# Kernel optimization log

Measured on AMD Instinct MI355X. Metric: run time of the kernel, lower is better.

The kernel has to match this reference:

```python
import jax, jax.numpy as jnp
import numpy as np

N, E, F_IN, H, C = 100000, 1250000, 512, 64, 40
K = 2


def _lin_w(key, fan_out, fan_in):
    bound = 1.0 / np.sqrt(fan_in)
    return jax.random.uniform(key, (fan_out, fan_in), jnp.float32, -bound, bound)


def setup_inputs() -> dict:
    key = jax.random.key(0)
    ks = jax.random.split(key, 14)
    x = jax.random.normal(ks[0], (N, F_IN), dtype=jnp.float32)
    edge_index = jax.random.randint(ks[1], (2, E), 0, N, dtype=jnp.int64)
    inp = {
        "x": x,
        "edge_index": edge_index,
        "W_in": _lin_w(ks[2], H, F_IN),
        "b_in": jnp.zeros((H,), jnp.float32),
        "W1_0": _lin_w(ks[3], H, H),
        "W2_0": _lin_w(ks[4], H, H),
        "Wf_0": _lin_w(ks[5], H, H),
        "W1_1": _lin_w(ks[6], H, H),
        "W2_1": _lin_w(ks[7], H, H),
        "Wf_1": _lin_w(ks[8], H, H),
        "W_out": _lin_w(ks[9], C, H),
        "b_out": jnp.zeros((C,), jnp.float32),
    }
    return inp


def _step_conv(Q, row, col, W1, W2, Wf, n):
    # StepConv.forward with step == 0 (the only valid branch in the source)
    h3 = Q @ W1.T              # [N, H]
    h4 = Q @ W2.T              # [N, H]
    hloop = jax.nn.relu(Q @ Wf.T)
    # edge gate: s = sigmoid(-<h3[row], h4[col]>)  per edge
    s = jax.nn.sigmoid(-jnp.sum(h3[row] * h4[col], axis=1))  # [E]
    # propagate (source_to_target): scatter messages from row into col
    agg3 = jax.ops.segment_sum(s[:, None] * h3[row], col, num_segments=n)
    agg4 = jax.ops.segment_sum((1.0 - s)[:, None] * h4[row], col, num_segments=n)
    return hloop + agg3 - agg4


def reference(x, edge_index, W_in, b_in, W1_0, W2_0, Wf_0, W1_1, W2_1, Wf_1, W_out, b_out):
    n = x.shape[0]
    row, col = edge_index[0], edge_index[1]
    Q = x @ W_in.T + b_in
    for (W1, W2, Wf) in ((W1_0, W2_0, Wf_0), (W1_1, W2_1, Wf_1)):
        hq3 = _step_conv(Q, row, col, W1, W2, Wf, n)
        # F.normalize(p=2, dim=1), eps=1e-12
        Q = hq3 / jnp.maximum(jnp.linalg.norm(hq3, axis=1, keepdims=True), 1e-12)
    logits = Q @ W_out.T + b_out
    return jax.nn.log_softmax(logits, axis=1)
```

## Files before the change

### kernel.cpp

```cpp
#include <hip/hip_runtime.h>
#include <hip/hip_bf16.h>
#include <math.h>

#define H 64
#define FIN 512
#define COUT 40

typedef __attribute__((ext_vector_type(8))) short bf16x8;
typedef __attribute__((ext_vector_type(4))) float f32x4;

__device__ __forceinline__ unsigned short f2bf(float f) {
    union { float f; unsigned u; } v; v.f = f;
    unsigned r = v.u + 0x7FFF + ((v.u >> 16) & 1);
    return (unsigned short)(r >> 16);
}
__device__ __forceinline__ float bflo(unsigned u) { return __uint_as_float(u << 16); }
__device__ __forceinline__ float bfhi(unsigned u) { return __uint_as_float(u & 0xffff0000u); }

__global__ void k_pack(const float* __restrict__ W_in,
                       const float* __restrict__ W1_0, const float* __restrict__ W2_0,
                       const float* __restrict__ Wf_0,
                       const float* __restrict__ W1_1, const float* __restrict__ W2_1,
                       const float* __restrict__ Wf_1,
                       const float* __restrict__ W_out,
                       uint4* __restrict__ Bp, uint4* __restrict__ Bc0,
                       uint4* __restrict__ Bc1, uint4* __restrict__ Bo) {
    int t = blockIdx.x * blockDim.x + threadIdx.x;
    const float* src;
    uint4* dst;
    if (t < 4096) {
        int kb = t >> 6, n = t & 63;
        src = &W_in[n * FIN + kb * 8];
        dst = &Bp[t];
    } else if (t < 4096 + 1536) {
        int u = t - 4096;
        int j = u >> 9, kb = (u >> 6) & 7, n = u & 63;
        const float* W = (j == 0) ? W1_0 : (j == 1) ? W2_0 : Wf_0;
        src = &W[n * H + kb * 8];
        dst = &Bc0[u];
    } else if (t < 4096 + 3072) {
        int u = t - 4096 - 1536;
        int j = u >> 9, kb = (u >> 6) & 7, n = u & 63;
        const float* W = (j == 0) ? W1_1 : (j == 1) ? W2_1 : Wf_1;
        src = &W[n * H + kb * 8];
        dst = &Bc1[u];
    } else if (t < 4096 + 3072 + 512) {
        int u = t - 4096 - 3072;
        int kb = u >> 6, col = u & 63;
        if (col >= COUT) { Bo[u] = make_uint4(0u, 0u, 0u, 0u); return; }
        src = &W_out[col * H + kb * 8];
        dst = &Bo[u];
    } else return;
    float4 a0 = *(const float4*)&src[0];
    float4 a1 = *(const float4*)&src[4];
    uint4 u;
    u.x = ((unsigned)f2bf(a0.y) << 16) | f2bf(a0.x);
    u.y = ((unsigned)f2bf(a0.w) << 16) | f2bf(a0.z);
    u.z = ((unsigned)f2bf(a1.y) << 16) | f2bf(a1.x);
    u.w = ((unsigned)f2bf(a1.w) << 16) | f2bf(a1.z);
    *dst = u;
}

__global__ void k_zero(int* __restrict__ p, int n) {
    int i = blockIdx.x * blockDim.x + threadIdx.x;
    if (i < n) p[i] = 0;
}

__global__ void k_hist(const int* __restrict__ ei, int* __restrict__ deg, int nE) {
    int e = blockIdx.x * blockDim.x + threadIdx.x;
    if (e < nE) atomicAdd(&deg[ei[nE + e]], 1);
}

__global__ __launch_bounds__(256) void k_scan1(const int* __restrict__ deg, int* __restrict__ epos,
                                               int* __restrict__ blocksum, int n) {
    __shared__ int tmp[256];
    int t = threadIdx.x;
    int base = blockIdx.x * 1024 + t * 4;
    int v[4]; int s = 0;
#pragma unroll
    for (int i = 0; i < 4; ++i) { v[i] = (base + i < n) ? deg[base + i] : 0; s += v[i]; }
    tmp[t] = s;
    __syncthreads();
    int incl = s;
    for (int off = 1; off < 256; off <<= 1) {
        int y = (t >= off) ? tmp[t - off] : 0;
        __syncthreads();
        incl += y;
        tmp[t] = incl;
        __syncthreads();
    }
    if (t == 255) blocksum[blockIdx.x] = incl;
    int run = incl - s;
#pragma unroll
    for (int i = 0; i < 4; ++i) { if (base + i < n) epos[base + i] = run; run += v[i]; }
}

__global__ __launch_bounds__(256) void k_scan2(const int* __restrict__ blocksum,
                                               int* __restrict__ blockoff, int nb) {
    __shared__ int tmp[256];
    int t = threadIdx.x;
    int s = (t < nb) ? blocksum[t] : 0;
    tmp[t] = s;
    __syncthreads();
    int incl = s;
    for (int off = 1; off < 256; off <<= 1) {
        int y = (t >= off) ? tmp[t - off] : 0;
        __syncthreads();
        incl += y;
        tmp[t] = incl;
        __syncthreads();
    }
    if (t < nb) blockoff[t] = incl - s;
}

__global__ __launch_bounds__(256) void k_scan3(int* __restrict__ epos, const int* __restrict__ blockoff,
                                               int* __restrict__ cursor, int n, int nE) {
    int b = blockIdx.x;
    int off = blockoff[b];
    int base = b * 1024 + threadIdx.x * 4;
#pragma unroll
    for (int i = 0; i < 4; ++i) {
        if (base + i < n) {
            int p = epos[base + i] + off;
            epos[base + i] = p;
            cursor[base + i] = p;
        }
    }
    if (b == 0 && threadIdx.x == 0) epos[n] = nE;
}

__global__ void k_scatter(const int* __restrict__ ei, int* __restrict__ cursor,
                          int* __restrict__ srcidx, int nE) {
    int e = blockIdx.x * blockDim.x + threadIdx.x;
    if (e < nE) {
        int c = ei[nE + e];
        int p = atomicAdd(&cursor[c], 1);
        srcidx[p] = ei[e];
    }
}

__global__ __launch_bounds__(256) void k_in_gemm(
    const float* __restrict__ x, const uint4* __restrict__ Bp,
    const float* __restrict__ bias, unsigned short* __restrict__ qbf, int n) {
    __shared__ uint4 As4[256];
    __shared__ uint4 Bs4[256];
    int tid = threadIdx.x;
    int base = blockIdx.x * 64;
    int lane = tid & 63, w = tid >> 6;

    int srow = tid >> 2;
    int sg = tid & 3;
    int sgs = sg ^ ((srow >> 1) & 3);
    bool rowok = (base + srow) < n;
    const float* xsrc = &x[(size_t)(base + srow) * FIN + sg * 8];

    int arow = 16 * w + (lane & 15);
    int ag = (lane >> 4) ^ ((arow >> 1) & 3);
    int aidx = arow * 4 + ag;
    int kg = lane >> 4;

    f32x4 acc[4];
#pragma unroll
    for (int i = 0; i < 4; ++i) acc[i] = (f32x4){0.f, 0.f, 0.f, 0.f};

    for (int kk = 0; kk < FIN; kk += 32) {
        float4 a0 = make_float4(0.f, 0.f, 0.f, 0.f), a1 = a0;
        if (rowok) {
            a0 = *(const float4*)&xsrc[kk];
            a1 = *(const float4*)&xsrc[kk + 4];
        }
        uint4 bstage = Bp[((kk >> 3) + (tid >> 6)) * 64 + (tid & 63)];
        __syncthreads();
        {
            uint4 u;
            u.x = ((unsigned)f2bf(a0.y) << 16) | f2bf(a0.x);
            u.y = ((unsigned)f2bf(a0.w) << 16) | f2bf(a0.z);
            u.z = ((unsigned)f2bf(a1.y) << 16) | f2bf(a1.x);
            u.w = ((unsigned)f2bf(a1.w) << 16) | f2bf(a1.z);
            As4[srow * 4 + sgs] = u;
            Bs4[tid] = bstage;
        }
        __syncthreads();
        bf16x8 af = *(const bf16x8*)&As4[aidx];
#pragma unroll
        for (int nt = 0; nt < 4; ++nt) {
            bf16x8 bfr = *(const bf16x8*)&Bs4[kg * 64 + nt * 16 + (lane & 15)];
            acc[nt] = __builtin_amdgcn_mfma_f32_16x16x32_bf16(af, bfr, acc[nt], 0, 0, 0);
        }
    }
    int col0 = lane & 15, rowg = lane >> 4;
#pragma unroll
    for (int nt = 0; nt < 4; ++nt) {
        float bv = bias[nt * 16 + col0];
#pragma unroll
        for (int reg = 0; reg < 4; ++reg) {
            int r = base + 16 * w + rowg * 4 + reg;
            if (r < n) qbf[(size_t)r * H + nt * 16 + col0] = f2bf(acc[nt][reg] + bv);
        }
    }
}

__global__ __launch_bounds__(256) void k_layer_gemm(
    const uint4* __restrict__ Qbf, const uint4* __restrict__ Bc,
    unsigned* __restrict__ P, unsigned short* __restrict__ hl, int n) {
    __shared__ uint4 Qs[512];
    int tid = threadIdx.x;
    int base = blockIdx.x * 64;
    int lane = tid & 63, w = tid >> 6;
    {
        int r = tid >> 2, g0 = (tid & 3) * 2;
        uint4 u0 = make_uint4(0u, 0u, 0u, 0u), u1 = u0;
        if (base + r < n) {
            u0 = Qbf[(size_t)(base + r) * 8 + g0];
            u1 = Qbf[(size_t)(base + r) * 8 + g0 + 1];
        }
        Qs[r * 8 + (g0 ^ (r & 7))] = u0;
        Qs[r * 8 + ((g0 + 1) ^ (r & 7))] = u1;
    }
    __syncthreads();

    int arow = w * 16 + (lane & 15);
    f32x4 acc[12];
#pragma unroll
    for (int i = 0; i < 12; ++i) acc[i] = (f32x4){0.f, 0.f, 0.f, 0.f};

#pragma unroll
    for (int ks = 0; ks < 2; ++ks) {
        int g = ks * 4 + (lane >> 4);
        bf16x8 af = *(const bf16x8*)&Qs[arow * 8 + (g ^ (arow & 7))];
#pragma unroll
        for (int j = 0; j < 3; ++j) {
#pragma unroll
            for (int nt = 0; nt < 4; ++nt) {
                bf16x8 bfr = *(const bf16x8*)&Bc[(j * 8 + g) * 64 + nt * 16 + (lane & 15)];
                acc[j * 4 + nt] = __builtin_amdgcn_mfma_f32_16x16x32_bf16(af, bfr, acc[j * 4 + nt], 0, 0, 0);
            }
        }
    }
    int col0 = lane & 15, rowg = lane >> 4;
#pragma unroll
    for (int nt = 0; nt < 4; ++nt) {
#pragma unroll
        for (int reg = 0; reg < 4; ++reg) {
            int r = base + w * 16 + rowg * 4 + reg;
            if (r < n) {
                int col = nt * 16 + col0;
                unsigned pv = ((unsigned)f2bf(acc[4 + nt][reg]) << 16) | f2bf(acc[nt][reg]);
                P[(size_t)r * H + col] = pv;
                hl[(size_t)r * H + col] = f2bf(fmaxf(acc[8 + nt][reg], 0.f));
            }
        }
    }
}

__global__ __launch_bounds__(256) void k_agg(
    const int* __restrict__ rowptr, const int* __restrict__ srcidx,
    const unsigned* __restrict__ P, const unsigned* __restrict__ hl32,
    unsigned* __restrict__ Qbf32, int n) {
    int tid = threadIdx.x;
    int lane = tid & 63;
    int w = tid >> 6;
    int c = blockIdx.x * 4 + w;
    if (c >= n) return;
    int q = lane >> 4;
    int j = lane & 15;
    const uint4* P4 = (const uint4*)P;

    uint4 pc = P4[(size_t)c * 16 + j];
    float4 h4c = make_float4(bfhi(pc.x), bfhi(pc.y), bfhi(pc.z), bfhi(pc.w));
    float4 acc = make_float4(0.f, 0.f, 0.f, 0.f);

    int k0 = rowptr[c], k1 = rowptr[c + 1];
    if (k0 < k1) {
        const uint4 Z = make_uint4(0u, 0u, 0u, 0u);
        int last = k1 - 1;
        int e0 = k0 + q;
        int sA = srcidx[min(e0, last)];
        bool vA = e0 < k1;
        int sB = srcidx[min(e0 + 4, last)];
        bool vB = (e0 + 4) < k1;
        uint4 pA = P4[(size_t)sA * 16 + j];
        if (!vA) pA = Z;

        for (int kb = k0; kb < k1; kb += 4) {
            int e2 = kb + 8 + q;
            int sC = srcidx[min(e2, last)];
            bool vC = e2 < k1;
            uint4 pB = P4[(size_t)sB * 16 + j];
            if (!vB) pB = Z;
            float4 h3r = make_float4(bflo(pA.x), bflo(pA.y), bflo(pA.z), bflo(pA.w));
            float4 h4r = make_float4(bfhi(pA.x), bfhi(pA.y), bfhi(pA.z), bfhi(pA.w));
            float d = h3r.x * h4c.x + h3r.y * h4c.y + h3r.z * h4c.z + h3r.w * h4c.w;
            d += __shfl_xor(d, 1, 64);
            d += __shfl_xor(d, 2, 64);
            d += __shfl_xor(d, 4, 64);
            d += __shfl_xor(d, 8, 64);
            float s = 1.0f / (1.0f + __expf(d));
            float t = 1.0f - s;
            acc.x += s * h3r.x - t * h4r.x;
            acc.y += s * h3r.y - t * h4r.y;
            acc.z += s * h3r.z - t * h4r.z;
            acc.w += s * h3r.w - t * h4r.w;
            pA = pB; sB = sC; vB = vC;
        }
    }
    acc.x += __shfl_xor(acc.x, 16, 64);
    acc.y += __shfl_xor(acc.y, 16, 64);
    acc.z += __shfl_xor(acc.z, 16, 64);
    acc.w += __shfl_xor(acc.w, 16, 64);
    acc.x += __shfl_xor(acc.x, 32, 64);
    acc.y += __shfl_xor(acc.y, 32, 64);
    acc.z += __shfl_xor(acc.z, 32, 64);
    acc.w += __shfl_xor(acc.w, 32, 64);

    uint2 hv = *(const uint2*)&hl32[(size_t)c * 32 + j * 2];
    acc.x += bflo(hv.x); acc.y += bfhi(hv.x);
    acc.z += bflo(hv.y); acc.w += bfhi(hv.y);

    float ss = acc.x * acc.x + acc.y * acc.y + acc.z * acc.z + acc.w * acc.w;
    ss += __shfl_xor(ss, 1, 64);
    ss += __shfl_xor(ss, 2, 64);
    ss += __shfl_xor(ss, 4, 64);
    ss += __shfl_xor(ss, 8, 64);
    float inv = 1.0f / fmaxf(sqrtf(ss), 1e-12f);

    if (lane < 16) {
        uint2 o;
        o.x = ((unsigned)f2bf(acc.y * inv) << 16) | f2bf(acc.x * inv);
        o.y = ((unsigned)f2bf(acc.w * inv) << 16) | f2bf(acc.z * inv);
        *(uint2*)&Qbf32[(size_t)c * 32 + j * 2] = o;
    }
}

__global__ __launch_bounds__(256) void k_head(
    const uint4* __restrict__ Qbf, const uint4* __restrict__ Bo,
    const float* __restrict__ b_out, float* __restrict__ out, int n) {
    __shared__ uint4 Qs[512];
    int tid = threadIdx.x;
    int base = blockIdx.x * 64;
    int lane = tid & 63, w = tid >> 6;
    {
        int r = tid >> 2, g0 = (tid & 3) * 2;
        uint4 u0 = make_uint4(0u, 0u, 0u, 0u), u1 = u0;
        if (base + r < n) {
            u0 = Qbf[(size_t)(base + r) * 8 + g0];
            u1 = Qbf[(size_t)(base + r) * 8 + g0 + 1];
        }
        Qs[r * 8 + (g0 ^ (r & 7))] = u0;
        Qs[r * 8 + ((g0 + 1) ^ (r & 7))] = u1;
    }
    __syncthreads();

    int arow = w * 16 + (lane & 15);
    f32x4 acc[3];
#pragma unroll
    for (int i = 0; i < 3; ++i) acc[i] = (f32x4){0.f, 0.f, 0.f, 0.f};
#pragma unroll
    for (int ks = 0; ks < 2; ++ks) {
        int g = ks * 4 + (lane >> 4);
        bf16x8 af = *(const bf16x8*)&Qs[arow * 8 + (g ^ (arow & 7))];
#pragma unroll
        for (int nt = 0; nt < 3; ++nt) {
            bf16x8 bfr = *(const bf16x8*)&Bo[g * 64 + nt * 16 + (lane & 15)];
            acc[nt] = __builtin_amdgcn_mfma_f32_16x16x32_bf16(af, bfr, acc[nt], 0, 0, 0);
        }
    }
    int col = lane & 15, rowg = lane >> 4;
    float bv0 = b_out[col];
    float bv1 = b_out[16 + col];
    float bv2 = (col < 8) ? b_out[32 + col] : 0.f;
#pragma unroll
    for (int reg = 0; reg < 4; ++reg) {
        int r = base + w * 16 + rowg * 4 + reg;
        float v0 = acc[0][reg] + bv0;
        float v1 = acc[1][reg] + bv1;
        float v2 = (col < 8) ? (acc[2][reg] + bv2) : -3.0e38f;
        float m = fmaxf(fmaxf(v0, v1), v2);
        m = fmaxf(m, __shfl_xor(m, 1, 64));
        m = fmaxf(m, __shfl_xor(m, 2, 64));
        m = fmaxf(m, __shfl_xor(m, 4, 64));
        m = fmaxf(m, __shfl_xor(m, 8, 64));
        float ex = __expf(v0 - m) + __expf(v1 - m) + ((col < 8) ? __expf(v2 - m) : 0.f);
        ex += __shfl_xor(ex, 1, 64);
        ex += __shfl_xor(ex, 2, 64);
        ex += __shfl_xor(ex, 4, 64);
        ex += __shfl_xor(ex, 8, 64);
        float lse = m + logf(ex);
        if (r < n) {
            out[(size_t)r * COUT + col] = v0 - lse;
            out[(size_t)r * COUT + 16 + col] = v1 - lse;
            if (col < 8) out[(size_t)r * COUT + 32 + col] = v2 - lse;
        }
    }
}

extern "C" void kernel_launch(void* const* d_in, const int* in_sizes, int n_in,
                              void* d_out, int out_size, void* d_ws, size_t ws_size,
                              hipStream_t stream) {
    const float* x     = (const float*)d_in[0];
    const int*   ei    = (const int*)d_in[1];
    const float* W_in  = (const float*)d_in[2];
    const float* b_in  = (const float*)d_in[3];
    const float* W1_0  = (const float*)d_in[4];
    const float* W2_0  = (const float*)d_in[5];
    const float* Wf_0  = (const float*)d_in[6];
    const float* W1_1  = (const float*)d_in[7];
    const float* W2_1  = (const float*)d_in[8];
    const float* Wf_1  = (const float*)d_in[9];
    const float* W_out = (const float*)d_in[10];
    const float* b_out = (const float*)d_in[11];
    float* out = (float*)d_out;

    int N = in_sizes[0] / FIN;
    int E = in_sizes[1] / 2;

    uint4* Bp    = (uint4*)d_ws;
    uint4* Bc0   = Bp + 4096;
    uint4* Bc1   = Bc0 + 1536;
    uint4* Bo    = Bc1 + 1536;
    unsigned* Qbf32 = (unsigned*)(Bo + 512);
    unsigned* P  = Qbf32 + (size_t)N * 32;
    unsigned* hl32 = P + (size_t)N * H;
    int* rowptr  = (int*)(hl32 + (size_t)N * 32);
    int* deg     = rowptr + (N + 2);
    int* cursor  = deg + N;
    int* srcidx  = cursor + N;
    int* blocksum = srcidx + E;
    int* blockoff = blocksum + 256;

    k_pack<<<30, 256, 0, stream>>>(W_in, W1_0, W2_0, Wf_0, W1_1, W2_1, Wf_1, W_out,
                                   Bp, Bc0, Bc1, Bo);

    int nb = (N + 1023) / 1024;
    k_zero<<<(N + 255) / 256, 256, 0, stream>>>(deg, N);
    k_hist<<<(E + 255) / 256, 256, 0, stream>>>(ei, deg, E);
    k_scan1<<<nb, 256, 0, stream>>>(deg, rowptr, blocksum, N);
    k_scan2<<<1, 256, 0, stream>>>(blocksum, blockoff, nb);
    k_scan3<<<nb, 256, 0, stream>>>(rowptr, blockoff, cursor, N, E);
    k_scatter<<<(E + 255) / 256, 256, 0, stream>>>(ei, cursor, srcidx, E);

    int gm = (N + 63) / 64;
    k_in_gemm<<<gm, 256, 0, stream>>>(x, Bp, b_in, (unsigned short*)Qbf32, N);

    int ga = (N + 3) / 4;
    k_layer_gemm<<<gm, 256, 0, stream>>>((const uint4*)Qbf32, Bc0, P, (unsigned short*)hl32, N);
    k_agg<<<ga, 256, 0, stream>>>(rowptr, srcidx, P, hl32, Qbf32, N);
    k_layer_gemm<<<gm, 256, 0, stream>>>((const uint4*)Qbf32, Bc1, P, (unsigned short*)hl32, N);
    k_agg<<<ga, 256, 0, stream>>>(rowptr, srcidx, P, hl32, Qbf32, N);
    k_head<<<gm, 256, 0, stream>>>((const uint4*)Qbf32, Bo, b_out, out, N);
}
```

Before: 352.6 us.

## Double K-tile in input GEMM, use fast rcp/rsq intrinsics, memset degrees

The input GEMM now processes 64 K-elements per iteration instead of 32, with wider loads, larger shared tiles and an XOR swizzle over 8 groups. This halves the number of barrier pairs and raises the bytes in flight per thread while streaming x. The aggregation kernel replaces the exact division in the sigmoid with a hardware reciprocal, and replaces the normalisation sqrt+divide with an rsq clamped at 1e12. The degree-zeroing kernel becomes hipMemsetAsync. The approximate intrinsics slightly change numerics, and the larger tiles increase LDS use per block.

```diff
diff --git a/kernel.cpp b/kernel.cpp
--- a/kernel.cpp
+++ b/kernel.cpp
@@ -61,11 +61,6 @@
     *dst = u;
 }
 
-__global__ void k_zero(int* __restrict__ p, int n) {
-    int i = blockIdx.x * blockDim.x + threadIdx.x;
-    if (i < n) p[i] = 0;
-}
-
 __global__ void k_hist(const int* __restrict__ ei, int* __restrict__ deg, int nE) {
     int e = blockIdx.x * blockDim.x + threadIdx.x;
     if (e < nE) atomicAdd(&deg[ei[nE + e]], 1);
@@ -142,53 +137,64 @@
 __global__ __launch_bounds__(256) void k_in_gemm(
     const float* __restrict__ x, const uint4* __restrict__ Bp,
     const float* __restrict__ bias, unsigned short* __restrict__ qbf, int n) {
-    __shared__ uint4 As4[256];
-    __shared__ uint4 Bs4[256];
+    __shared__ uint4 As4[512];
+    __shared__ uint4 Bs4[512];
     int tid = threadIdx.x;
     int base = blockIdx.x * 64;
     int lane = tid & 63, w = tid >> 6;
 
     int srow = tid >> 2;
-    int sg = tid & 3;
-    int sgs = sg ^ ((srow >> 1) & 3);
+    int g0 = (tid & 3) * 2;
     bool rowok = (base + srow) < n;
-    const float* xsrc = &x[(size_t)(base + srow) * FIN + sg * 8];
+    const float* xsrc = &x[(size_t)(base + srow) * FIN + g0 * 8];
 
     int arow = 16 * w + (lane & 15);
-    int ag = (lane >> 4) ^ ((arow >> 1) & 3);
-    int aidx = arow * 4 + ag;
     int kg = lane >> 4;
+    int l15 = lane & 15;
 
     f32x4 acc[4];
 #pragma unroll
     for (int i = 0; i < 4; ++i) acc[i] = (f32x4){0.f, 0.f, 0.f, 0.f};
 
-    for (int kk = 0; kk < FIN; kk += 32) {
-        float4 a0 = make_float4(0.f, 0.f, 0.f, 0.f), a1 = a0;
+    for (int kk = 0; kk < FIN; kk += 64) {
+        float4 a0 = make_float4(0.f,0.f,0.f,0.f), a1 = a0, a2 = a0, a3 = a0;
         if (rowok) {
             a0 = *(const float4*)&xsrc[kk];
             a1 = *(const float4*)&xsrc[kk + 4];
-        }
-        uint4 bstage = Bp[((kk >> 3) + (tid >> 6)) * 64 + (tid & 63)];
+            a2 = *(const float4*)&xsrc[kk + 8];
+            a3 = *(const float4*)&xsrc[kk + 12];
+        }
+        uint4 b0 = Bp[(kk >> 3) * 64 + tid];
+        uint4 b1 = Bp[(kk >> 3) * 64 + tid + 256];
         __syncthreads();
         {
-            uint4 u;
-            u.x = ((unsigned)f2bf(a0.y) << 16) | f2bf(a0.x);
-            u.y = ((unsigned)f2bf(a0.w) << 16) | f2bf(a0.z);
-            u.z = ((unsigned)f2bf(a1.y) << 16) | f2bf(a1.x);
-            u.w = ((unsigned)f2bf(a1.w) << 16) | f2bf(a1.z);
-            As4[srow * 4 + sgs] = u;
-            Bs4[tid] = bstage;
-        }
-        __syncthreads();
-        bf16x8 af = *(const bf16x8*)&As4[aidx];
-#pragma unroll
-        for (int nt = 0; nt < 4; ++nt) {
-            bf16x8 bfr = *(const bf16x8*)&Bs4[kg * 64 + nt * 16 + (lane & 15)];
-            acc[nt] = __builtin_amdgcn_mfma_f32_16x16x32_bf16(af, bfr, acc[nt], 0, 0, 0);
-        }
-    }
-    int col0 = lane & 15, rowg = lane >> 4;
+            uint4 u0, u1;
+            u0.x = ((unsigned)f2bf(a0.y) << 16) | f2bf(a0.x);
+            u0.y = ((unsigned)f2bf(a0.w) << 16) | f2bf(a0.z);
+            u0.z = ((unsigned)f2bf(a1.y) << 16) | f2bf(a1.x);
+            u0.w = ((unsigned)f2bf(a1.w) << 16) | f2bf(a1.z);
+            u1.x = ((unsigned)f2bf(a2.y) << 16) | f2bf(a2.x);
+            u1.y = ((unsigned)f2bf(a2.w) << 16) | f2bf(a2.z);
+            u1.z = ((unsigned)f2bf(a3.y) << 16) | f2bf(a3.x);
+            u1.w = ((unsigned)f2bf(a3.w) << 16) | f2bf(a3.z);
+            As4[srow * 8 + (g0 ^ (srow & 7))] = u0;
+            As4[srow * 8 + ((g0 + 1) ^ (srow & 7))] = u1;
+            Bs4[tid] = b0;
+            Bs4[tid + 256] = b1;
+        }
+        __syncthreads();
+#pragma unroll
+        for (int ks = 0; ks < 2; ++ks) {
+            int g = ks * 4 + kg;
+            bf16x8 af = *(const bf16x8*)&As4[arow * 8 + (g ^ (arow & 7))];
+#pragma unroll
+            for (int nt = 0; nt < 4; ++nt) {
+                bf16x8 bfr = *(const bf16x8*)&Bs4[g * 64 + nt * 16 + l15];
+                acc[nt] = __builtin_amdgcn_mfma_f32_16x16x32_bf16(af, bfr, acc[nt], 0, 0, 0);
+            }
+        }
+    }
+    int col0 = l15, rowg = lane >> 4;
 #pragma unroll
     for (int nt = 0; nt < 4; ++nt) {
         float bv = bias[nt * 16 + col0];
@@ -295,7 +301,7 @@
             d += __shfl_xor(d, 2, 64);
             d += __shfl_xor(d, 4, 64);
             d += __shfl_xor(d, 8, 64);
-            float s = 1.0f / (1.0f + __expf(d));
+            float s = __builtin_amdgcn_rcpf(1.0f + __expf(d));
             float t = 1.0f - s;
             acc.x += s * h3r.x - t * h4r.x;
             acc.y += s * h3r.y - t * h4r.y;
@@ -322,7 +328,7 @@
     ss += __shfl_xor(ss, 2, 64);
     ss += __shfl_xor(ss, 4, 64);
     ss += __shfl_xor(ss, 8, 64);
-    float inv = 1.0f / fmaxf(sqrtf(ss), 1e-12f);
+    float inv = fminf(__builtin_amdgcn_rsqf(ss), 1e12f);
 
     if (lane < 16) {
         uint2 o;
@@ -432,7 +438,7 @@
                                    Bp, Bc0, Bc1, Bo);
 
     int nb = (N + 1023) / 1024;
-    k_zero<<<(N + 255) / 256, 256, 0, stream>>>(deg, N);
+    hipMemsetAsync(deg, 0, (size_t)N * sizeof(int), stream);
     k_hist<<<(E + 255) / 256, 256, 0, stream>>>(ei, deg, E);
     k_scan1<<<nb, 256, 0, stream>>>(deg, rowptr, blocksum, N);
     k_scan2<<<1, 256, 0, stream>>>(blocksum, blockoff, nb);
```

New measurement: 362.7 us. +2.8%, slower.
